# Kernel tuning notes

Measured on AMD Instinct MI355X. Metric: run time of the kernel, lower is better.

## Reference

```python
import jax, jax.numpy as jnp
import numpy as np

B, T, D, H = 4, 2048, 1024, 16
HD = D // H  # 64

def setup_inputs() -> dict:
    key = jax.random.key(0)
    k1, k2, k3 = jax.random.split(key, 3)
    scale = 1.0 / np.sqrt(D)
    x = jax.random.normal(k1, (B, T, D), dtype=jnp.float32)
    w_qkv = jax.random.normal(k2, (D, 3 * D), dtype=jnp.float32) * scale
    w_o = jax.random.normal(k3, (D, D), dtype=jnp.float32) * scale
    return {"x": x, "w_qkv": w_qkv, "w_o": w_o}

def reference(x, w_qkv, w_o):
    b, t, d = x.shape
    qkv = jnp.einsum('btd,de->bte', x, w_qkv)  # [B,T,3D]
    q, k, v = jnp.split(qkv, 3, axis=-1)
    # [B,H,T,hd]
    q = q.reshape(b, t, H, HD).transpose(0, 2, 1, 3)
    k = k.reshape(b, t, H, HD).transpose(0, 2, 1, 3)
    v = v.reshape(b, t, H, HD).transpose(0, 2, 1, 3)
    scores = jnp.einsum('bhqd,bhkd->bhqk', q, k) * (1.0 / jnp.sqrt(jnp.asarray(HD, x.dtype)))
    causal = jnp.tril(jnp.ones((t, t), dtype=bool))
    scores = jnp.where(causal[None, None, :, :], scores, -jnp.inf)
    weights = jax.nn.softmax(scores, axis=-1)
    out = jnp.einsum('bhqk,bhkd->bhqd', weights, v)
    out = out.transpose(0, 2, 1, 3).reshape(b, t, d)
    return jnp.einsum('btd,de->bte', out, w_o)
```

## Files before the change

### kernel.cpp

```cpp
#include <hip/hip_runtime.h>
#include <hip/hip_bf16.h>
#include <stdint.h>

#define HD 64
#define NH 16
#define TT 2048
#define DD 1024

typedef uint16_t u16;
typedef __bf16 bf16_t;
typedef bf16_t bf16x8 __attribute__((ext_vector_type(8)));
typedef float f32x4 __attribute__((ext_vector_type(4)));

__device__ __forceinline__ u16 f2b(float f) {
    union { float f; uint32_t u; } v; v.f = f;
    uint32_t u = v.u;
    u += 0x7fff + ((u >> 16) & 1);
    return (u16)(u >> 16);
}

__device__ __forceinline__ u16 b16(float f) {
    union { __bf16 h; u16 u; } c; c.h = (__bf16)f; return c.u;
}

__device__ __forceinline__ void gload16(const void* g, void* l) {
    __builtin_amdgcn_global_load_lds(
        (__attribute__((address_space(1))) void*)g,
        (__attribute__((address_space(3))) void*)l, 16, 0, 0);
}


__global__ void f32_to_bf16_vec(const float* __restrict__ in, u16* __restrict__ out, int n4) {
    int i = blockIdx.x * 256 + threadIdx.x;
    if (i >= n4) return;
    float4 v = ((const float4*)in)[i];
    ushort4 r;
    r.x = f2b(v.x); r.y = f2b(v.y); r.z = f2b(v.z); r.w = f2b(v.w);
    ((ushort4*)out)[i] = r;
}

__global__ void transpose_f32_bf16(const float* __restrict__ in, u16* __restrict__ out, int R, int C) {
    __shared__ float tile[32][33];
    const int tx = threadIdx.x, ty = threadIdx.y;
    const int c0 = blockIdx.x * 32, r0 = blockIdx.y * 32;
#pragma unroll
    for (int j = 0; j < 32; j += 8)
        tile[ty + j][tx] = in[(size_t)(r0 + ty + j) * C + c0 + tx];
    __syncthreads();
#pragma unroll
    for (int j = 0; j < 32; j += 8)
        out[(size_t)(c0 + ty + j) * R + r0 + tx] = f2b(tile[tx][ty + j]);
}


template<int MODE>
__global__ __launch_bounds__(512, 4)
void gemm9(const u16* __restrict__ A, const u16* __restrict__ Bt,
           int N, int K, int nwg,
           u16* __restrict__ oq, u16* __restrict__ ok, u16* __restrict__ ovT,
           float* __restrict__ of)
{
    __shared__ __align__(16) u16 As[3][256 * 32];
    __shared__ __align__(16) u16 Bs[3][128 * 32];
    const int tid = threadIdx.x;
    const int lane = tid & 63, l15 = lane & 15, g = lane >> 4;
    const int wid = tid >> 6, wm = wid >> 1, wn = wid & 1;

    const int gx = N >> 7;
    const int cpx = nwg >> 3;
    const int sid = (blockIdx.x & 7) * cpx + (blockIdx.x >> 3);
    const long row0 = (long)(sid / gx) * 256;
    const long col0 = (long)(sid % gx) * 128;

    const u16* Ag = A + row0 * K;
    const u16* Bg = Bt + col0 * K;

    const f32x4 z4 = {0.f, 0.f, 0.f, 0.f};
    f32x4 acc[4][4];
#pragma unroll
    for (int i = 0; i < 4; i++)
#pragma unroll
        for (int n = 0; n < 4; n++) acc[i][n] = z4;

    const int swz = (l15 >> 1) & 3;

#define STG(t_, s_) do { const int ko = (t_) << 5;                                                 \
        { const int c = tid;       const int r_ = c >> 2;                                          \
          gload16(Ag + (size_t)r_ * K + ko + ((((c & 3) ^ ((r_ >> 1) & 3))) << 3), &As[s_][c << 3]); } \
        { const int c = tid + 512; const int r_ = c >> 2;                                          \
          gload16(Ag + (size_t)r_ * K + ko + ((((c & 3) ^ ((r_ >> 1) & 3))) << 3), &As[s_][c << 3]); } \
        { const int c = tid;       const int r_ = c >> 2;                                          \
          gload16(Bg + (size_t)r_ * K + ko + ((((c & 3) ^ ((r_ >> 1) & 3))) << 3), &Bs[s_][c << 3]); } \
    } while (0)

    const int NT = K >> 5;
    STG(0, 0);
    STG(1, 1);
    int sc = 0;
    for (int t = 0; t < NT; ++t) {
        if (t < NT - 1) asm volatile("s_waitcnt vmcnt(3)" ::: "memory");
        else            asm volatile("s_waitcnt vmcnt(0)" ::: "memory");
        __builtin_amdgcn_s_barrier();
        bf16x8 af[4], bfr[4];
#pragma unroll
        for (int m = 0; m < 4; m++)
            af[m]  = *(const bf16x8*)&As[sc][(wm * 64 + m * 16 + l15) * 32 + ((g ^ swz) << 3)];
#pragma unroll
        for (int n = 0; n < 4; n++)
            bfr[n] = *(const bf16x8*)&Bs[sc][(wn * 64 + n * 16 + l15) * 32 + ((g ^ swz) << 3)];
        const int sn = (sc == 0) ? 2 : sc - 1;
        if (t + 2 < NT) STG(t + 2, sn);
        __builtin_amdgcn_s_setprio(1);
#pragma unroll
        for (int m = 0; m < 4; m++)
#pragma unroll
            for (int n = 0; n < 4; n++)
                acc[m][n] = __builtin_amdgcn_mfma_f32_16x16x32_bf16(af[m], bfr[n], acc[m][n], 0, 0, 0);
        __builtin_amdgcn_s_setprio(0);
        sc = (sc == 2) ? 0 : sc + 1;
    }
#undef STG

    if (MODE == 0) {
        const int which = (int)(col0 >> 10);
        const long b = row0 >> 11;
#pragma unroll
        for (int m = 0; m < 4; m++) {
            const long r = row0 + wm * 64 + m * 16 + g * 4;
            const long t = r & (TT - 1);
#pragma unroll
            for (int n = 0; n < 4; n++) {
                const long c = col0 + wn * 64 + n * 16 + l15;
                const int h  = (int)((c >> 6) & 15);
                const int hd = (int)(c & 63);
                if (which == 0) {
#pragma unroll
                    for (int e = 0; e < 4; e++)
                        oq[((b * NH + h) * TT + t + e) * HD + hd] = f2b(acc[m][n][e] * 0.125f);
                } else if (which == 1) {
#pragma unroll
                    for (int e = 0; e < 4; e++)
                        ok[((b * NH + h) * TT + t + e) * HD + hd] = f2b(acc[m][n][e]);
                } else {
                    ushort4 pk;
                    pk.x = f2b(acc[m][n][0]); pk.y = f2b(acc[m][n][1]);
                    pk.z = f2b(acc[m][n][2]); pk.w = f2b(acc[m][n][3]);
                    *(ushort4*)&ovT[((b * NH + h) * HD + hd) * TT + t] = pk;
                }
            }
        }
    } else {
#pragma unroll
        for (int m = 0; m < 4; m++) {
            const long r = row0 + wm * 64 + m * 16 + g * 4;
#pragma unroll
            for (int n = 0; n < 4; n++) {
                const long c = col0 + wn * 64 + n * 16 + l15;
#pragma unroll
                for (int e = 0; e < 4; e++)
                    of[(r + e) * (long)N + c] = acc[m][n][e];
            }
        }
    }
}


__global__ __launch_bounds__(256, 3)
void attn_fwd(const u16* __restrict__ gq, const u16* __restrict__ gk,
              const u16* __restrict__ gvT, u16* __restrict__ o)
{
    __shared__ __align__(16) u16 Klds[2][64 * 64];
    __shared__ __align__(16) u16 Vlds[2][64 * 64];
    __shared__ __align__(16) u16 Plds[4][32 * 64];

    const int tid = threadIdx.x;
    const int wv = tid >> 6, lane = tid & 63, l15 = lane & 15, g = lane >> 4;
    const int bh = blockIdx.x & 63;
    const int qt = 15 - (blockIdx.x >> 6);
    const int q0 = qt * 128;
    const int qw0 = q0 + wv * 32;

    const u16* qbase = gq + (size_t)bh * TT * HD;
    const u16* kbase = gk + (size_t)bh * TT * HD;
    const u16* vbase = gvT + (size_t)bh * HD * TT;

    const float NEG_INF = -__builtin_inff();
    const f32x4 z4 = {0.f, 0.f, 0.f, 0.f};

    bf16x8 qf[2][2];
#pragma unroll
    for (int qi = 0; qi < 2; qi++)
#pragma unroll
        for (int hs = 0; hs < 2; hs++)
            qf[qi][hs] = *(const bf16x8*)(qbase + (size_t)(qw0 + qi * 16 + l15) * HD + hs * 32 + g * 8);

    f32x4 o_acc[2][4];
    float m[2], ls[2];
#pragma unroll
    for (int qi = 0; qi < 2; qi++) {
#pragma unroll
        for (int n = 0; n < 4; n++) o_acc[qi][n] = z4;
        m[qi] = NEG_INF; ls[qi] = 0.f;
    }

    const int r0_ = tid >> 3, c0_ = tid & 7;
    const int r1_ = (tid + 256) >> 3, c1_ = (tid + 256) & 7;

#define STAGE(buf, k0s)                                                                    \
    do {                                                                                   \
        gload16(kbase + (size_t)((k0s) + r0_) * HD + ((c0_ ^ (r0_ & 7)) * 8), &Klds[buf][tid * 8]);          \
        gload16(kbase + (size_t)((k0s) + r1_) * HD + ((c1_ ^ (r1_ & 7)) * 8), &Klds[buf][(tid + 256) * 8]);  \
        gload16(vbase + (size_t)r0_ * TT + (k0s) + ((c0_ ^ (r0_ & 7)) * 8), &Vlds[buf][tid * 8]);            \
        gload16(vbase + (size_t)r1_ * TT + (k0s) + ((c1_ ^ (r1_ & 7)) * 8), &Vlds[buf][(tid + 256) * 8]);    \
    } while (0)

    const int nkt = q0 / 64 + 2;
    STAGE(0, 0);
    for (int kt = 0; kt < nkt; ++kt) {
        const int k0 = kt * 64;
        const int cur = kt & 1;
        if (kt + 1 < nkt) {
            STAGE(cur ^ 1, k0 + 64);
            asm volatile("s_waitcnt vmcnt(4)" ::: "memory");
        } else {
            asm volatile("s_waitcnt vmcnt(0)" ::: "memory");
        }
        __builtin_amdgcn_s_barrier();
        if (k0 <= qw0 + 31) {
            const int sw = l15 & 7;
            f32x4 s2[2][4];
            __builtin_amdgcn_s_setprio(1);
#pragma unroll
            for (int kb = 0; kb < 4; kb++) {
                bf16x8 kf0 = *(const bf16x8*)&Klds[cur][(kb * 16 + l15) * 64 + ((g ^ sw) * 8)];
                bf16x8 kf1 = *(const bf16x8*)&Klds[cur][(kb * 16 + l15) * 64 + (((4 + g) ^ sw) * 8)];
#pragma unroll
                for (int qi = 0; qi < 2; qi++) {
                    f32x4 t0 = __builtin_amdgcn_mfma_f32_16x16x32_bf16(kf0, qf[qi][0], z4, 0, 0, 0);
                    s2[qi][kb] = __builtin_amdgcn_mfma_f32_16x16x32_bf16(kf1, qf[qi][1], t0, 0, 0, 0);
                }
            }
            __builtin_amdgcn_s_setprio(0);
            if (k0 + 63 > qw0) {
#pragma unroll
                for (int qi = 0; qi < 2; qi++)
#pragma unroll
                    for (int kb = 0; kb < 4; kb++)
#pragma unroll
                        for (int e = 0; e < 4; e++) {
                            const int kk = k0 + kb * 16 + g * 4 + e;
                            const int qq = qw0 + qi * 16 + l15;
                            if (kk > qq) s2[qi][kb][e] = NEG_INF;
                        }
            }
#pragma unroll
            for (int qi = 0; qi < 2; qi++) {
                f32x4 mx = s2[qi][0];
#pragma unroll
                for (int kb = 1; kb < 4; kb++)
#pragma unroll
                    for (int e = 0; e < 4; e++) mx[e] = fmaxf(mx[e], s2[qi][kb][e]);
                float pmax = fmaxf(fmaxf(mx[0], mx[1]), fmaxf(mx[2], mx[3]));
                pmax = fmaxf(pmax, __shfl_xor(pmax, 16));
                pmax = fmaxf(pmax, __shfl_xor(pmax, 32));
                float mn = m[qi];
                const int resc = !__all(pmax <= mn + 8.f);
                if (resc) {
                    const float mold = mn;
                    mn = fmaxf(mold, pmax);
                    m[qi] = mn;
                    const float sc = __expf(mold - mn);
                    ls[qi] *= sc;
#pragma unroll
                    for (int e = 0; e < 4; e++) {
                        const float sce = __shfl(sc, (lane & 48) + (((lane >> 4) & 3) << 2) + e);
#pragma unroll
                        for (int n = 0; n < 4; n++) o_acc[qi][n][e] *= sce;
                    }
                }
                const int prow = qi * 16 + l15;
                u16* pb = &Plds[wv][prow * 64];
                float rsum = 0.f;
#pragma unroll
                for (int kb = 0; kb < 4; kb++) {
                    const float p0 = __expf(s2[qi][kb][0] - mn);
                    const float p1 = __expf(s2[qi][kb][1] - mn);
                    const float p2 = __expf(s2[qi][kb][2] - mn);
                    const float p3 = __expf(s2[qi][kb][3] - mn);
                    rsum += (p0 + p1) + (p2 + p3);
                    ushort4 pk;
                    pk.x = b16(p0); pk.y = b16(p1); pk.z = b16(p2); pk.w = b16(p3);
                    *(ushort4*)&pb[(((kb << 2) + g) ^ l15) * 4] = pk;
                }
                rsum += __shfl_xor(rsum, 16);
                rsum += __shfl_xor(rsum, 32);
                ls[qi] += rsum;
            }
#pragma unroll
            for (int ks = 0; ks < 2; ks++) {
                bf16x8 vf[4];
#pragma unroll
                for (int n = 0; n < 4; n++)
                    vf[n] = *(const bf16x8*)&Vlds[cur][(n * 16 + l15) * 64 + (((ks * 4 + g) ^ sw) * 8)];
                __builtin_amdgcn_s_setprio(1);
#pragma unroll
                for (int qi = 0; qi < 2; qi++) {
                    const u16* pb = &Plds[wv][(qi * 16 + l15) * 64];
                    const int G0 = ((ks << 3) + (g << 1)) ^ l15;
                    const int G1 = ((ks << 3) + (g << 1) + 1) ^ l15;
                    const uint2 ra = *(const uint2*)&pb[G0 * 4];
                    const uint2 rb = *(const uint2*)&pb[G1 * 4];
                    union { uint32_t w[4]; bf16x8 v; } pu;
                    pu.w[0] = ra.x; pu.w[1] = ra.y; pu.w[2] = rb.x; pu.w[3] = rb.y;
#pragma unroll
                    for (int n = 0; n < 4; n++)
                        o_acc[qi][n] = __builtin_amdgcn_mfma_f32_16x16x32_bf16(pu.v, vf[n], o_acc[qi][n], 0, 0, 0);
                }
                __builtin_amdgcn_s_setprio(0);
            }
        }
        __builtin_amdgcn_s_barrier();
    }
#undef STAGE

    const int b = bh >> 4, h = bh & 15;
#pragma unroll
    for (int qi = 0; qi < 2; qi++) {
        const float linv = 1.f / ls[qi];
#pragma unroll
        for (int e = 0; e < 4; e++) {
            const float inv = __shfl(linv, (lane & 48) + (((lane >> 4) & 3) << 2) + e);
            const int t = qw0 + qi * 16 + g * 4 + e;
#pragma unroll
            for (int n = 0; n < 4; n++)
                o[((size_t)(b * TT + t)) * DD + h * HD + n * 16 + l15] = f2b(o_acc[qi][n][e] * inv);
        }
    }
}


extern "C" void kernel_launch(void* const* d_in, const int* in_sizes, int n_in,
                              void* d_out, int out_size, void* d_ws, size_t ws_size,
                              hipStream_t stream)
{
    const float* x     = (const float*)d_in[0];
    const float* w_qkv = (const float*)d_in[1];
    const float* w_o   = (const float*)d_in[2];
    float* out = (float*)d_out;
    char* ws = (char*)d_ws;

    u16* xb    = (u16*)(ws);
    u16* wqkvT = (u16*)(ws + 16777216);
    u16* woT   = (u16*)(ws + 23068672);
    u16* wsq   = (u16*)(ws + 25165824);
    u16* wsk   = (u16*)(ws + 41943040);
    u16* wsvT  = (u16*)(ws + 58720256);
    u16* attno = (u16*)(ws + 75497472);

    f32_to_bf16_vec<<<8192, 256, 0, stream>>>(x, xb, 2097152);
    dim3 tb(32, 8);
    transpose_f32_bf16<<<dim3(96, 32), tb, 0, stream>>>(w_qkv, wqkvT, 1024, 3072);
    transpose_f32_bf16<<<dim3(32, 32), tb, 0, stream>>>(w_o,   woT,   1024, 1024);

    gemm9<0><<<768, 512, 0, stream>>>(xb, wqkvT, 3072, 1024, 768, wsq, wsk, wsvT, nullptr);
    attn_fwd<<<1024, 256, 0, stream>>>(wsq, wsk, wsvT, attno);
    gemm9<1><<<256, 512, 0, stream>>>(attno, woT, 1024, 1024, 256, nullptr, nullptr, nullptr, out);
}
```

Measured before the change: 164.3 us.

## Load K/V directly from global into registers per wave, drop LDS staging and barriers

Replaces the block-wide double-buffered LDS staging of K and V with per-wave direct global loads into registers. Each wave now iterates only over its own causal range, and all block barriers are removed. It also folds log2(e) into the Q scale so softmax can use exp2f, and remaps block indices so consecutive blocks spread across heads for L2 locality. The cost is that four waves each fetch the same K/V tiles from global/L2 with no cross-wave sharing, and global load latency is exposed without software prefetch.

```diff
diff --git a/kernel.cpp b/kernel.cpp
--- a/kernel.cpp
+++ b/kernel.cpp
@@ -136,7 +136,7 @@
                 if (which == 0) {
 #pragma unroll
                     for (int e = 0; e < 4; e++)
-                        oq[((b * NH + h) * TT + t + e) * HD + hd] = f2b(acc[m][n][e] * 0.125f);
+                        oq[((b * NH + h) * TT + t + e) * HD + hd] = f2b(acc[m][n][e] * 0.18033688f);
                 } else if (which == 1) {
 #pragma unroll
                     for (int e = 0; e < 4; e++)
@@ -169,16 +169,15 @@
 void attn_fwd(const u16* __restrict__ gq, const u16* __restrict__ gk,
               const u16* __restrict__ gvT, u16* __restrict__ o)
 {
-    __shared__ __align__(16) u16 Klds[2][64 * 64];
-    __shared__ __align__(16) u16 Vlds[2][64 * 64];
     __shared__ __align__(16) u16 Plds[4][32 * 64];
 
     const int tid = threadIdx.x;
     const int wv = tid >> 6, lane = tid & 63, l15 = lane & 15, g = lane >> 4;
-    const int bh = blockIdx.x & 63;
-    const int qt = 15 - (blockIdx.x >> 6);
-    const int q0 = qt * 128;
-    const int qw0 = q0 + wv * 32;
+    const int blk = blockIdx.x;
+    const int j = blk >> 3;
+    const int bh = (blk & 7) * 8 + (j & 7);
+    const int qt = 15 - (j >> 3);
+    const int qw0 = qt * 128 + wv * 32;
 
     const u16* qbase = gq + (size_t)bh * TT * HD;
     const u16* kbase = gk + (size_t)bh * TT * HD;
@@ -203,125 +202,116 @@
         m[qi] = NEG_INF; ls[qi] = 0.f;
     }
 
-    const int r0_ = tid >> 3, c0_ = tid & 7;
-    const int r1_ = (tid + 256) >> 3, c1_ = (tid + 256) & 7;
-
-#define STAGE(buf, k0s)                                                                    \
-    do {                                                                                   \
-        gload16(kbase + (size_t)((k0s) + r0_) * HD + ((c0_ ^ (r0_ & 7)) * 8), &Klds[buf][tid * 8]);          \
-        gload16(kbase + (size_t)((k0s) + r1_) * HD + ((c1_ ^ (r1_ & 7)) * 8), &Klds[buf][(tid + 256) * 8]);  \
-        gload16(vbase + (size_t)r0_ * TT + (k0s) + ((c0_ ^ (r0_ & 7)) * 8), &Vlds[buf][tid * 8]);            \
-        gload16(vbase + (size_t)r1_ * TT + (k0s) + ((c1_ ^ (r1_ & 7)) * 8), &Vlds[buf][(tid + 256) * 8]);    \
-    } while (0)
-
-    const int nkt = q0 / 64 + 2;
-    STAGE(0, 0);
+    const int nkt = (qw0 + 31) / 64 + 1;
     for (int kt = 0; kt < nkt; ++kt) {
         const int k0 = kt * 64;
-        const int cur = kt & 1;
-        if (kt + 1 < nkt) {
-            STAGE(cur ^ 1, k0 + 64);
-            asm volatile("s_waitcnt vmcnt(4)" ::: "memory");
-        } else {
-            asm volatile("s_waitcnt vmcnt(0)" ::: "memory");
-        }
-        __builtin_amdgcn_s_barrier();
-        if (k0 <= qw0 + 31) {
-            const int sw = l15 & 7;
-            f32x4 s2[2][4];
-            __builtin_amdgcn_s_setprio(1);
+        bf16x8 kf0[4], kf1[4];
+#pragma unroll
+        for (int kb = 0; kb < 4; kb++) {
+            const u16* kr = kbase + (size_t)(k0 + kb * 16 + l15) * HD + g * 8;
+            kf0[kb] = *(const bf16x8*)(kr);
+            kf1[kb] = *(const bf16x8*)(kr + 32);
+        }
+        f32x4 s2[2][4];
+        __builtin_amdgcn_s_setprio(1);
+#pragma unroll
+        for (int kb = 0; kb < 4; kb++)
+#pragma unroll
+            for (int qi = 0; qi < 2; qi++) {
+                f32x4 t0 = __builtin_amdgcn_mfma_f32_16x16x32_bf16(kf0[kb], qf[qi][0], z4, 0, 0, 0);
+                s2[qi][kb] = __builtin_amdgcn_mfma_f32_16x16x32_bf16(kf1[kb], qf[qi][1], t0, 0, 0, 0);
+            }
+        __builtin_amdgcn_s_setprio(0);
+        bf16x8 vf0[4], vf1[4];
+#pragma unroll
+        for (int n = 0; n < 4; n++) {
+            const u16* vr = vbase + (size_t)(n * 16 + l15) * TT + k0 + g * 8;
+            vf0[n] = *(const bf16x8*)(vr);
+            vf1[n] = *(const bf16x8*)(vr + 32);
+        }
+        if (k0 + 63 > qw0) {
+#pragma unroll
+            for (int qi = 0; qi < 2; qi++)
+#pragma unroll
+                for (int kb = 0; kb < 4; kb++)
+#pragma unroll
+                    for (int e = 0; e < 4; e++) {
+                        const int kk = k0 + kb * 16 + g * 4 + e;
+                        const int qq = qw0 + qi * 16 + l15;
+                        if (kk > qq) s2[qi][kb][e] = NEG_INF;
+                    }
+        }
+#pragma unroll
+        for (int qi = 0; qi < 2; qi++) {
+            f32x4 mx = s2[qi][0];
+#pragma unroll
+            for (int kb = 1; kb < 4; kb++)
+#pragma unroll
+                for (int e = 0; e < 4; e++) mx[e] = fmaxf(mx[e], s2[qi][kb][e]);
+            float pmax = fmaxf(fmaxf(mx[0], mx[1]), fmaxf(mx[2], mx[3]));
+            pmax = fmaxf(pmax, __shfl_xor(pmax, 16));
+            pmax = fmaxf(pmax, __shfl_xor(pmax, 32));
+            float mn = m[qi];
+            const int resc = !__all(pmax <= mn + 11.541560f);
+            if (resc) {
+                const float mold = mn;
+                mn = fmaxf(mold, pmax);
+                m[qi] = mn;
+                const float sc = exp2f(mold - mn);
+                ls[qi] *= sc;
+#pragma unroll
+                for (int e = 0; e < 4; e++) {
+                    const float sce = __shfl(sc, (lane & 48) + (((lane >> 4) & 3) << 2) + e);
+#pragma unroll
+                    for (int n = 0; n < 4; n++) o_acc[qi][n][e] *= sce;
+                }
+            }
+            const int prow = qi * 16 + l15;
+            u16* pb = &Plds[wv][prow * 64];
+            float rsum = 0.f;
 #pragma unroll
             for (int kb = 0; kb < 4; kb++) {
-                bf16x8 kf0 = *(const bf16x8*)&Klds[cur][(kb * 16 + l15) * 64 + ((g ^ sw) * 8)];
-                bf16x8 kf1 = *(const bf16x8*)&Klds[cur][(kb * 16 + l15) * 64 + (((4 + g) ^ sw) * 8)];
-#pragma unroll
-                for (int qi = 0; qi < 2; qi++) {
-                    f32x4 t0 = __builtin_amdgcn_mfma_f32_16x16x32_bf16(kf0, qf[qi][0], z4, 0, 0, 0);
-                    s2[qi][kb] = __builtin_amdgcn_mfma_f32_16x16x32_bf16(kf1, qf[qi][1], t0, 0, 0, 0);
-                }
-            }
-            __builtin_amdgcn_s_setprio(0);
-            if (k0 + 63 > qw0) {
-#pragma unroll
-                for (int qi = 0; qi < 2; qi++)
-#pragma unroll
-                    for (int kb = 0; kb < 4; kb++)
-#pragma unroll
-                        for (int e = 0; e < 4; e++) {
-                            const int kk = k0 + kb * 16 + g * 4 + e;
-                            const int qq = qw0 + qi * 16 + l15;
-                            if (kk > qq) s2[qi][kb][e] = NEG_INF;
-                        }
-            }
-#pragma unroll
-            for (int qi = 0; qi < 2; qi++) {
-                f32x4 mx = s2[qi][0];
-#pragma unroll
-                for (int kb = 1; kb < 4; kb++)
-#pragma unroll
-                    for (int e = 0; e < 4; e++) mx[e] = fmaxf(mx[e], s2[qi][kb][e]);
-                float pmax = fmaxf(fmaxf(mx[0], mx[1]), fmaxf(mx[2], mx[3]));
-                pmax = fmaxf(pmax, __shfl_xor(pmax, 16));
-                pmax = fmaxf(pmax, __shfl_xor(pmax, 32));
-                float mn = m[qi];
-                const int resc = !__all(pmax <= mn + 8.f);
-                if (resc) {
-                    const float mold = mn;
-                    mn = fmaxf(mold, pmax);
-                    m[qi] = mn;
-                    const float sc = __expf(mold - mn);
-                    ls[qi] *= sc;
-#pragma unroll
-                    for (int e = 0; e < 4; e++) {
-                        const float sce = __shfl(sc, (lane & 48) + (((lane >> 4) & 3) << 2) + e);
-#pragma unroll
-                        for (int n = 0; n < 4; n++) o_acc[qi][n][e] *= sce;
-                    }
-                }
-                const int prow = qi * 16 + l15;
-                u16* pb = &Plds[wv][prow * 64];
-                float rsum = 0.f;
-#pragma unroll
-                for (int kb = 0; kb < 4; kb++) {
-                    const float p0 = __expf(s2[qi][kb][0] - mn);
-                    const float p1 = __expf(s2[qi][kb][1] - mn);
-                    const float p2 = __expf(s2[qi][kb][2] - mn);
-                    const float p3 = __expf(s2[qi][kb][3] - mn);
-                    rsum += (p0 + p1) + (p2 + p3);
-                    ushort4 pk;
-                    pk.x = b16(p0); pk.y = b16(p1); pk.z = b16(p2); pk.w = b16(p3);
-                    *(ushort4*)&pb[(((kb << 2) + g) ^ l15) * 4] = pk;
-                }
-                rsum += __shfl_xor(rsum, 16);
-                rsum += __shfl_xor(rsum, 32);
-                ls[qi] += rsum;
-            }
-#pragma unroll
-            for (int ks = 0; ks < 2; ks++) {
-                bf16x8 vf[4];
+                const float p0 = exp2f(s2[qi][kb][0] - mn);
+                const float p1 = exp2f(s2[qi][kb][1] - mn);
+                const float p2 = exp2f(s2[qi][kb][2] - mn);
+                const float p3 = exp2f(s2[qi][kb][3] - mn);
+                rsum += (p0 + p1) + (p2 + p3);
+                ushort4 pk;
+                pk.x = b16(p0); pk.y = b16(p1); pk.z = b16(p2); pk.w = b16(p3);
+                *(ushort4*)&pb[(((kb << 2) + g) ^ l15) * 4] = pk;
+            }
+            rsum += __shfl_xor(rsum, 16);
+            rsum += __shfl_xor(rsum, 32);
+            ls[qi] += rsum;
+        }
+        asm volatile("s_waitcnt lgkmcnt(0)" ::: "memory");
+        __builtin_amdgcn_s_setprio(1);
+#pragma unroll
+        for (int qi = 0; qi < 2; qi++) {
+            const u16* pb = &Plds[wv][(qi * 16 + l15) * 64];
+            {
+                const int G0 = ((g << 1)) ^ l15, G1 = ((g << 1) + 1) ^ l15;
+                const uint2 ra = *(const uint2*)&pb[G0 * 4];
+                const uint2 rb = *(const uint2*)&pb[G1 * 4];
+                union { uint32_t w[4]; bf16x8 v; } pu;
+                pu.w[0] = ra.x; pu.w[1] = ra.y; pu.w[2] = rb.x; pu.w[3] = rb.y;
 #pragma unroll
                 for (int n = 0; n < 4; n++)
-                    vf[n] = *(const bf16x8*)&Vlds[cur][(n * 16 + l15) * 64 + (((ks * 4 + g) ^ sw) * 8)];
-                __builtin_amdgcn_s_setprio(1);
-#pragma unroll
-                for (int qi = 0; qi < 2; qi++) {
-                    const u16* pb = &Plds[wv][(qi * 16 + l15) * 64];
-                    const int G0 = ((ks << 3) + (g << 1)) ^ l15;
-                    const int G1 = ((ks << 3) + (g << 1) + 1) ^ l15;
-                    const uint2 ra = *(const uint2*)&pb[G0 * 4];
-                    const uint2 rb = *(const uint2*)&pb[G1 * 4];
-                    union { uint32_t w[4]; bf16x8 v; } pu;
-                    pu.w[0] = ra.x; pu.w[1] = ra.y; pu.w[2] = rb.x; pu.w[3] = rb.y;
-#pragma unroll
-                    for (int n = 0; n < 4; n++)
-                        o_acc[qi][n] = __builtin_amdgcn_mfma_f32_16x16x32_bf16(pu.v, vf[n], o_acc[qi][n], 0, 0, 0);
-                }
-                __builtin_amdgcn_s_setprio(0);
-            }
-        }
-        __builtin_amdgcn_s_barrier();
-    }
-#undef STAGE
+                    o_acc[qi][n] = __builtin_amdgcn_mfma_f32_16x16x32_bf16(pu.v, vf0[n], o_acc[qi][n], 0, 0, 0);
+            }
+            {
+                const int G0 = (8 + (g << 1)) ^ l15, G1 = (8 + (g << 1) + 1) ^ l15;
+                const uint2 ra = *(const uint2*)&pb[G0 * 4];
+                const uint2 rb = *(const uint2*)&pb[G1 * 4];
+                union { uint32_t w[4]; bf16x8 v; } pu;
+                pu.w[0] = ra.x; pu.w[1] = ra.y; pu.w[2] = rb.x; pu.w[3] = rb.y;
+#pragma unroll
+                for (int n = 0; n < 4; n++)
+                    o_acc[qi][n] = __builtin_amdgcn_mfma_f32_16x16x32_bf16(pu.v, vf1[n], o_acc[qi][n], 0, 0, 0);
+            }
+        }
+        __builtin_amdgcn_s_setprio(0);
+    }
 
     const int b = bh >> 4, h = bh & 15;
 #pragma unroll
```

New measurement: 232.7 us. +41.6%, slower.
